# Kernel optimization log

Measured on AMD Instinct MI355X. Metric: run time of the kernel, lower is better.

Reference implementation:

```python
import jax, jax.numpy as jnp
import numpy as np

BS, N_LINKS, MAX_LEN = 8192, 512, 32
D_LINK, D_PATH, D_READ, N_OUT = 32, 128, 256, 3
BN_EPS = 1e-5


def setup_inputs() -> dict:
    key = jax.random.key(0)
    ks = jax.random.split(key, 16)
    capa = jax.random.uniform(ks[0], (BS, N_LINKS), jnp.float32, 0.5, 1.0) * 100.0
    avail = jax.random.uniform(ks[1], (BS, N_LINKS), jnp.float32) * capa
    loss = jax.random.uniform(ks[2], (BS, N_LINKS), jnp.float32) * 0.05
    demand = jax.random.uniform(ks[3], (BS,), jnp.float32) * 10.0
    path = jax.random.randint(ks[4], (BS, MAX_LEN), 0, N_LINKS)
    hop_num = jax.random.randint(ks[5], (BS,), 1, MAX_LEN + 1)
    s = 0.1
    inp = {
        "demand": demand,
        "link_avail_capacity": avail,
        "link_capacity": capa,
        "link_loss": loss,
        "path": path,
        "hop_num": hop_num,
        # GRU params (PyTorch layout: [3H, D] gates ordered r,z,n)
        "gru_w_ih": jax.random.normal(ks[6], (3 * D_PATH, D_LINK), jnp.float32) * s,
        "gru_w_hh": jax.random.normal(ks[7], (3 * D_PATH, D_PATH), jnp.float32) * s,
        "gru_b_ih": jax.random.normal(ks[8], (3 * D_PATH,), jnp.float32) * s,
        "gru_b_hh": jax.random.normal(ks[9], (3 * D_PATH,), jnp.float32) * s,
        "bn_gamma": jnp.ones((D_PATH,), jnp.float32),
        "bn_beta": jnp.zeros((D_PATH,), jnp.float32),
        # stacked readout heads [N_OUT, ...]
        "rW1": jax.random.normal(ks[10], (N_OUT, D_PATH, D_READ), jnp.float32) * s,
        "rb1": jnp.zeros((N_OUT, D_READ), jnp.float32),
        "rW2": jax.random.normal(ks[11], (N_OUT, D_READ, D_READ), jnp.float32) * s,
        "rb2": jnp.zeros((N_OUT, D_READ), jnp.float32),
        "rW3": jax.random.normal(ks[12], (N_OUT, D_READ, 1), jnp.float32) * s,
        "rb3": jnp.zeros((N_OUT, 1), jnp.float32),
    }
    return inp


def _gru_scan(x_bt, h0, w_ih, w_hh, b_ih, b_hh):
    # x_bt: [B, T, D]; h0: [B, H] -> outputs [B, T, H]
    H = h0.shape[-1]
    def step(h, x_t):
        gi = x_t @ w_ih.T + b_ih          # [B, 3H]
        gh = h @ w_hh.T + b_hh            # [B, 3H]
        i_r, i_z, i_n = gi[:, :H], gi[:, H:2*H], gi[:, 2*H:]
        h_r, h_z, h_n = gh[:, :H], gh[:, H:2*H], gh[:, 2*H:]
        r = jax.nn.sigmoid(i_r + h_r)
        z = jax.nn.sigmoid(i_z + h_z)
        n = jnp.tanh(i_n + r * h_n)
        h_new = (1.0 - z) * n + z * h
        return h_new, h_new
    _, outs = jax.lax.scan(step, h0, jnp.swapaxes(x_bt, 0, 1))
    return jnp.swapaxes(outs, 0, 1)


def reference(demand, link_avail_capacity, link_capacity, link_loss, path, hop_num,
              gru_w_ih, gru_w_hh, gru_b_ih, gru_b_hh, bn_gamma, bn_beta,
              rW1, rb1, rW2, rb2, rW3, rb3):
    bs, n_links = link_capacity.shape
    max_len = path.shape[1]
    max_capa = jax.lax.stop_gradient(jnp.max(link_capacity))
    # link_state: [B, n_links, D_LINK]; first D_LINK-4 channels are zeros
    feats = jnp.stack([
        link_avail_capacity / max_capa,
        link_capacity / max_capa,
        link_avail_capacity / link_capacity,
        link_loss,
    ], axis=-1)
    link_state = jnp.concatenate(
        [jnp.zeros((bs, n_links, D_LINK - 4), feats.dtype), feats], axis=-1)
    link_state = jax.lax.stop_gradient(link_state)  # original detaches
    # initial hidden: zeros except last channel = demand/max_capa
    h0 = jnp.concatenate(
        [jnp.zeros((bs, D_PATH - 1), feats.dtype), (demand / max_capa)[:, None]], axis=-1)
    # fused gather of link states along each path, masked past hop_num
    gathered = jnp.take_along_axis(link_state, path[:, :, None], axis=1)  # [B, T, D]
    mask = (jnp.arange(max_len)[None, :] < hop_num[:, None])[:, :, None]
    link_inputs = gathered * mask.astype(gathered.dtype)
    outputs = _gru_scan(link_inputs, h0, gru_w_ih, gru_w_hh, gru_b_ih, gru_b_hh)
    # extract hidden state at last hop of each path
    idx = (hop_num - 1)[:, None, None]
    flow = jnp.take_along_axis(outputs, idx, axis=1)[:, 0, :]  # [B, H]
    # BatchNorm1d (training mode: batch statistics, biased variance)
    mean = jnp.mean(flow, axis=0)
    var = jnp.mean((flow - mean) ** 2, axis=0)
    flow = (flow - mean) * jax.lax.rsqrt(var + BN_EPS) * bn_gamma + bn_beta
    # readout heads: Linear -> SELU -> Linear -> SELU -> Linear
    h1 = jax.nn.selu(jnp.einsum('bh,uhr->ubr', flow, rW1) + rb1[:, None, :])
    h2 = jax.nn.selu(jnp.einsum('ubr,urs->ubs', h1, rW2) + rb2[:, None, :])
    y = jnp.einsum('ubs,uso->ubo', h2, rW3) + rb3[:, None, :]  # [U, B, 1]
    return jnp.transpose(y[:, :, 0], (1, 0))  # [B, U]
```

## Files before the change

kernel.cpp:

```cpp
#include <hip/hip_runtime.h>


#define BS 8192
#define NL 512
#define ML 32
#define DP 128
#define DR 256
#define NJOB 512
#define ST 172

#define OFF_SUM    64
#define OFF_SSQ    192
#define OFF_CUR    576
#define OFF_PERM   640
#define OFF_WHH16  (OFF_PERM + BS)
#define OFF_W1     (OFF_WHH16 + 24576)
#define OFF_W2     (OFF_W1 + 49152)
#define OFF_FEATS  (OFF_W2 + 98304)
#define OFF_FLOW   (OFF_FEATS + BS*ML*4)

#define FEATS_BLOCKS 1024
#define MAX_BLOCKS   256
#define WPREP_BLOCKS 336
#define SORT_BID     (FEATS_BLOCKS + MAX_BLOCKS + WPREP_BLOCKS)
#define PREP_GRID    (SORT_BID + 1)

typedef _Float16 f16x8 __attribute__((ext_vector_type(8)));
typedef _Float16 f16x4 __attribute__((ext_vector_type(4)));
typedef float    f32x4 __attribute__((ext_vector_type(4)));

__device__ __forceinline__ float sigmoidf_(float x){
  return __builtin_amdgcn_rcpf(1.0f + __expf(-x));
}
__device__ __forceinline__ float tanhf_(float x){
  float t = __expf(2.0f*x);
  return 1.0f - 2.0f*__builtin_amdgcn_rcpf(1.0f + t);
}
__device__ __forceinline__ float seluf_(float x){
  const float sc = 1.0507009873554805f, al = 1.6732632423543772f;
  return x > 0.0f ? sc*x : sc*al*(__expf(x)-1.0f);
}

__global__ void prep_all(const int* __restrict__ path, const int* __restrict__ hop,
                         const float* __restrict__ avail, const float* __restrict__ capa,
                         const float* __restrict__ loss, const float* __restrict__ whh,
                         const float* __restrict__ rW1, const float* __restrict__ rW2,
                         float* ws){
  const int bid = blockIdx.x;
  const int tid = threadIdx.x;

  if (bid < FEATS_BLOCKS){
    int idx = bid*256 + tid;
    int b = idx >> 5, t = idx & 31;
    float4 f = make_float4(0.f, 0.f, 0.f, 0.f);
    if (t < hop[b]){
      int l = path[idx];
      float a = avail[b*NL + l];
      float c = capa [b*NL + l];
      f.x = a; f.y = c; f.z = a / c; f.w = loss[b*NL + l];
    }
    ((float4*)(ws + OFF_FEATS))[idx] = f;
  } else if (bid < FEATS_BLOCKS + MAX_BLOCKS){
    const float4* c4 = (const float4*)capa;
    const int n4 = BS*NL/4;
    float m = 0.0f;
    for (int i = (bid - FEATS_BLOCKS)*256 + tid; i < n4; i += MAX_BLOCKS*256){
      float4 v = c4[i];
      m = fmaxf(m, fmaxf(fmaxf(v.x, v.y), fmaxf(v.z, v.w)));
    }
    #pragma unroll
    for (int o = 32; o > 0; o >>= 1) m = fmaxf(m, __shfl_down(m, o, 64));
    if ((tid & 63) == 0) atomicMax((int*)ws, __float_as_int(m));
  } else if (bid < SORT_BID){
    _Float16* whh16 = (_Float16*)(ws + OFF_WHH16);
    _Float16* w1    = (_Float16*)(ws + OFF_W1);
    _Float16* w2    = (_Float16*)(ws + OFF_W2);
    int base = (bid - FEATS_BLOCKS - MAX_BLOCKS)*1024 + tid*4;
    if (base < 49152){
      const float4 v = *(const float4*)(whh + base);
      f16x4 o = { (_Float16)v.x, (_Float16)v.y, (_Float16)v.z, (_Float16)v.w };
      *(f16x4*)(whh16 + base) = o;
    } else if (base < 147456){
      int j = base - 49152; int u = j >> 15; int rem = j & 32767; int n = rem >> 7; int k = rem & 127;
      const float* src = rW1 + u*32768 + k*256 + n;
      f16x4 o = { (_Float16)src[0], (_Float16)src[256], (_Float16)src[512], (_Float16)src[768] };
      *(f16x4*)(w1 + j) = o;
    } else {
      int j = base - 147456; int u = j >> 16; int rem = j & 65535; int n = rem >> 8; int k = rem & 255;
      const float* src = rW2 + u*65536 + k*256 + n;
      f16x4 o = { (_Float16)src[0], (_Float16)src[256], (_Float16)src[512], (_Float16)src[768] };
      *(f16x4*)(w2 + j) = o;
    }
  } else {
    __shared__ int hist[32], start[32];
    for (int i = 64 + tid; i < 640; i += 256) ws[i] = 0.0f;
    if (tid < 32) hist[tid] = 0;
    __syncthreads();
    for (int b = tid; b < BS; b += 256) atomicAdd(&hist[32 - hop[b]], 1);
    __syncthreads();
    if (tid == 0){ int acc = 0; for (int i = 0; i < 32; ++i){ start[i] = acc; acc += hist[i]; } }
    __syncthreads();
    int* perm = (int*)ws + OFF_PERM;
    for (int b = tid; b < BS; b += 256){
      int pos = atomicAdd(&start[32 - hop[b]], 1);
      perm[pos] = b;
    }
  }
}

__launch_bounds__(512, 4)
__global__ void kgru(const float* __restrict__ demand, const int* __restrict__ hop,
                     const float* __restrict__ wih, const float* __restrict__ bih,
                     const float* __restrict__ bhh, float* __restrict__ ws,
                     float* __restrict__ flow){
  __shared__ _Float16 hA[2][16*ST];
  const int tid  = threadIdx.x;
  const int w    = tid >> 6;
  const int lane = tid & 63;
  const int lm   = lane & 15;
  const int qd   = lane >> 4;
  const int ch   = w*16 + lm;
  const float inv_maxc = 1.0f / ws[0];
  const int* perm = (const int*)ws + OFF_PERM;
  const float* feats = ws + OFF_FEATS;
  const _Float16* whh16 = (const _Float16*)(ws + OFF_WHH16);

  const int bid = blockIdx.x;
  const int q = (bid < 256) ? bid : 767 - bid;

  for (int idx = tid; idx < 1024; idx += 512){
    const int buf = idx >> 9;
    const int rem = idx & 511;
    const int m   = rem >> 5;
    const int c   = 128 + (rem & 31);
    hA[buf][m*ST + c] = (_Float16)0.f;
  }

  f16x8 bfr[5], bfz[5], bfnh[4], bfni;
  #pragma unroll
  for (int kc = 0; kc < 4; ++kc){
    bfr[kc]  = *(const f16x8*)(whh16 + (      ch)*128 + kc*32 + qd*8);
    bfz[kc]  = *(const f16x8*)(whh16 + (128 + ch)*128 + kc*32 + qd*8);
    bfnh[kc] = *(const f16x8*)(whh16 + (256 + ch)*128 + kc*32 + qd*8);
  }
  bfr[4] = (f16x8)0; bfz[4] = (f16x8)0; bfni = (f16x8)0;
  if (qd == 0){
    #pragma unroll
    for (int j = 0; j < 4; ++j){
      float s = (j < 2) ? inv_maxc : 1.0f;
      bfr[4][j] = (_Float16)(wih[(      ch)*32 + 28 + j] * s);
      bfz[4][j] = (_Float16)(wih[(128 + ch)*32 + 28 + j] * s);
      bfni[j]   = (_Float16)(wih[(256 + ch)*32 + 28 + j] * s);
    }
  }
  const float bR  = bih[ch]     + bhh[ch];
  const float bZ  = bih[128+ch] + bhh[128+ch];
  const float bNI = bih[256+ch];
  const float bNH = bhh[256+ch];

  int it[4], hp[4];
  #pragma unroll
  for (int r = 0; r < 4; ++r){
    it[r] = perm[q*16 + qd*4 + r];
    hp[r] = hop[it[r]];
  }
  int tmax = max(max(hp[0],hp[1]), max(hp[2],hp[3]));
  tmax = max(tmax, __shfl_xor(tmax, 16, 64));
  tmax = max(tmax, __shfl_xor(tmax, 32, 64));

  const int fw_i = w*2 + (lane >> 2);
  const int fw_c = lane & 3;
  const bool fw  = (lane < 8);
  const int  fw_b = fw ? perm[q*16 + fw_i] : 0;

  __syncthreads();

  float hprev[4];
  #pragma unroll
  for (int r = 0; r < 4; ++r){
    float h0 = (ch == 127) ? demand[it[r]] * inv_maxc : 0.0f;
    hprev[r] = h0;
    hA[0][(qd*4 + r)*ST + ch] = (_Float16)h0;
  }
  if (fw)
    hA[0][fw_i*ST + 128 + fw_c] = (_Float16)feats[(fw_b*ML + 0)*4 + fw_c];
  __syncthreads();

  for (int t = 0; t < tmax; ++t){
    const int cur = t & 1, nxt = cur ^ 1;
    if (fw && (t+1) < ML)
      hA[nxt][fw_i*ST + 128 + fw_c] = (_Float16)feats[(fw_b*ML + t + 1)*4 + fw_c];

    f32x4 accr  = {bR, bR, bR, bR};
    f32x4 accz  = {bZ, bZ, bZ, bZ};
    f32x4 accnh = {bNH, bNH, bNH, bNH};
    f32x4 accni = {bNI, bNI, bNI, bNI};
    #pragma unroll
    for (int kc = 0; kc < 5; ++kc){
      f16x8 a = *(const f16x8*)(&hA[cur][lm*ST + kc*32 + qd*8]);
      accr = __builtin_amdgcn_mfma_f32_16x16x32_f16(a, bfr[kc], accr, 0, 0, 0);
      accz = __builtin_amdgcn_mfma_f32_16x16x32_f16(a, bfz[kc], accz, 0, 0, 0);
      if (kc < 4)
        accnh = __builtin_amdgcn_mfma_f32_16x16x32_f16(a, bfnh[kc], accnh, 0, 0, 0);
      else
        accni = __builtin_amdgcn_mfma_f32_16x16x32_f16(a, bfni, accni, 0, 0, 0);
    }

    #pragma unroll
    for (int r = 0; r < 4; ++r){
      float rr = sigmoidf_(accr[r]);
      float zz = sigmoidf_(accz[r]);
      float nn = tanhf_(fmaf(rr, accnh[r], accni[r]));
      float hn = fmaf(zz, hprev[r] - nn, nn);
      if (t < hp[r]) hprev[r] = hn;
      hA[nxt][(qd*4 + r)*ST + ch] = (_Float16)hprev[r];
    }
    __syncthreads();
  }

  float ssum = 0.f, ssq = 0.f;
  #pragma unroll
  for (int r = 0; r < 4; ++r){
    float v = hprev[r];
    flow[it[r]*DP + ch] = v;
    ssum += v;
    ssq  = fmaf(v, v, ssq);
  }
  ssum += __shfl_xor(ssum, 16, 64);  ssum += __shfl_xor(ssum, 32, 64);
  ssq  += __shfl_xor(ssq,  16, 64);  ssq  += __shfl_xor(ssq,  32, 64);
  if (qd == 0){
    atomicAdd(&ws[OFF_SUM + ch], ssum);
    atomicAdd(&ws[OFF_SSQ + ch], ssq);
  }
}

__launch_bounds__(256, 4)
__global__ void kmlp(const float* __restrict__ flow, const float* __restrict__ ws,
                     const float* __restrict__ gamma, const float* __restrict__ beta,
                     const float* __restrict__ rb1, const float* __restrict__ rb2,
                     const float* __restrict__ rW3, const float* __restrict__ rb3,
                     float* __restrict__ out){
  __shared__ _Float16 x_lds[32*136];
  __shared__ _Float16 h1_lds[32*264];
  __shared__ float aa[DP], bb[DP];
  __shared__ float y_part[4][32];
  const int tid  = threadIdx.x;
  const int w    = tid >> 6;
  const int lane = tid & 63;
  const int lm   = lane & 15;
  const int qd   = lane >> 4;
  const int b0   = blockIdx.x * 32;
  const int u    = blockIdx.y;
  const _Float16* w1 = (const _Float16*)(ws + OFF_W1) + u*(DR*DP);
  const _Float16* w2 = (const _Float16*)(ws + OFF_W2) + u*(DR*DR);

  if (tid < DP){
    float m = ws[OFF_SUM + tid] * (1.0f/BS);
    float q = ws[OFF_SSQ + tid] * (1.0f/BS);
    float rstd = rsqrtf(q - m*m + 1e-5f);
    float a = rstd * gamma[tid];
    aa[tid] = a;
    bb[tid] = fmaf(-m, a, beta[tid]);
  }
  __syncthreads();

  for (int idx = tid; idx < 32*DP; idx += 256){
    int i = idx >> 7, h = idx & 127;
    x_lds[i*136 + h] = (_Float16)fmaf(flow[(b0 + i)*DP + h], aa[h], bb[h]);
  }
  __syncthreads();

  for (int nt = 0; nt < 4; ++nt){
    const int n = (4*w + nt)*16 + lm;
    const float bias1 = rb1[u*DR + n];
    f16x8 b1[4];
    #pragma unroll
    for (int kc = 0; kc < 4; ++kc)
      b1[kc] = *(const f16x8*)(w1 + n*DP + kc*32 + qd*8);
    #pragma unroll
    for (int mt = 0; mt < 2; ++mt){
      f32x4 acc = {bias1, bias1, bias1, bias1};
      #pragma unroll
      for (int kc = 0; kc < 4; ++kc){
        f16x8 a1 = *(const f16x8*)(&x_lds[(mt*16 + lm)*136 + kc*32 + qd*8]);
        acc = __builtin_amdgcn_mfma_f32_16x16x32_f16(a1, b1[kc], acc, 0, 0, 0);
      }
      #pragma unroll
      for (int r = 0; r < 4; ++r)
        h1_lds[(mt*16 + qd*4 + r)*264 + n] = (_Float16)seluf_(acc[r]);
    }
  }
  __syncthreads();

  {
    float p[2][4] = {{0.f,0.f,0.f,0.f},{0.f,0.f,0.f,0.f}};
    for (int nt = 0; nt < 4; ++nt){
      const int n = (4*w + nt)*16 + lm;
      const float bias2 = rb2[u*DR + n];
      const float w3l   = rW3[u*DR + n];
      f16x8 b2[8];
      #pragma unroll
      for (int kc = 0; kc < 8; ++kc)
        b2[kc] = *(const f16x8*)(w2 + n*DR + kc*32 + qd*8);
      #pragma unroll
      for (int mt = 0; mt < 2; ++mt){
        f32x4 acc = {bias2, bias2, bias2, bias2};
        #pragma unroll
        for (int kc = 0; kc < 8; ++kc){
          f16x8 a2 = *(const f16x8*)(&h1_lds[(mt*16 + lm)*264 + kc*32 + qd*8]);
          acc = __builtin_amdgcn_mfma_f32_16x16x32_f16(a2, b2[kc], acc, 0, 0, 0);
        }
        #pragma unroll
        for (int r = 0; r < 4; ++r)
          p[mt][r] += seluf_(acc[r]) * w3l;
      }
    }
    #pragma unroll
    for (int mt = 0; mt < 2; ++mt){
      #pragma unroll
      for (int r = 0; r < 4; ++r){
        float v = p[mt][r];
        v += __shfl_xor(v, 1, 64);
        v += __shfl_xor(v, 2, 64);
        v += __shfl_xor(v, 4, 64);
        v += __shfl_xor(v, 8, 64);
        if (lm == 0) y_part[w][mt*16 + qd*4 + r] = v;
      }
    }
  }
  __syncthreads();
  if (tid < 32){
    float y = y_part[0][tid] + y_part[1][tid] + y_part[2][tid] + y_part[3][tid] + rb3[u];
    out[(b0 + tid)*3 + u] = y;
  }
}

extern "C" void kernel_launch(void* const* d_in, const int* in_sizes, int n_in,
                              void* d_out, int out_size, void* d_ws, size_t ws_size,
                              hipStream_t stream){
  const float* demand = (const float*)d_in[0];
  const float* avail  = (const float*)d_in[1];
  const float* capa   = (const float*)d_in[2];
  const float* loss   = (const float*)d_in[3];
  const int*   path   = (const int*)d_in[4];
  const int*   hop    = (const int*)d_in[5];
  const float* wih    = (const float*)d_in[6];
  const float* whh    = (const float*)d_in[7];
  const float* bih    = (const float*)d_in[8];
  const float* bhh    = (const float*)d_in[9];
  const float* gamma  = (const float*)d_in[10];
  const float* beta   = (const float*)d_in[11];
  const float* rW1    = (const float*)d_in[12];
  const float* rb1    = (const float*)d_in[13];
  const float* rW2    = (const float*)d_in[14];
  const float* rb2    = (const float*)d_in[15];
  const float* rW3    = (const float*)d_in[16];
  const float* rb3    = (const float*)d_in[17];
  float* ws  = (float*)d_ws;
  float* out = (float*)d_out;

  prep_all <<<PREP_GRID, 256, 0, stream>>>(path, hop, avail, capa, loss,
                                           whh, rW1, rW2, ws);
  kgru     <<<NJOB, 512, 0, stream>>>(demand, hop, wih, bih, bhh, ws, ws + OFF_FLOW);
  kmlp     <<<dim3(BS/32, 3), 256, 0, stream>>>(ws + OFF_FLOW, ws, gamma, beta,
                                                rb1, rb2, rW3, rb3, out);
}
```

Measured before the change: 201.2 us.

## Fuse link-feature gather into GRU loop and pre-scale gate weights for exp2

Removes the separate feature-gather blocks from the prep kernel and the intermediate feats buffer. The GRU kernel now reads path indices and the avail/capa/loss values directly, software-pipelined two steps ahead, and computes avail/capa through lane shuffles. Separately, the W_hh, W_ih and bias terms are pre-scaled by -log2(e) or 2·log2(e), so sigmoid and tanh use exp2 directly without an extra multiply. This trades a workspace write and read pass for dependent global loads inside the sequential loop, which may add latency if the prefetch does not hide it.

Measured after the change: 207.0 us. +2.9%, slower.

```diff
diff --git a/kernel.cpp b/kernel.cpp
--- a/kernel.cpp
+++ b/kernel.cpp
@@ -19,22 +19,23 @@
 #define OFF_FEATS  (OFF_W2 + 98304)
 #define OFF_FLOW   (OFF_FEATS + BS*ML*4)
 
-#define FEATS_BLOCKS 1024
 #define MAX_BLOCKS   256
 #define WPREP_BLOCKS 336
-#define SORT_BID     (FEATS_BLOCKS + MAX_BLOCKS + WPREP_BLOCKS)
+#define SORT_BID     (MAX_BLOCKS + WPREP_BLOCKS)
 #define PREP_GRID    (SORT_BID + 1)
+
+#define KS (-1.44269504088896340736f)
+#define KT ( 2.88539008177792681472f)
 
 typedef _Float16 f16x8 __attribute__((ext_vector_type(8)));
 typedef _Float16 f16x4 __attribute__((ext_vector_type(4)));
 typedef float    f32x4 __attribute__((ext_vector_type(4)));
 
-__device__ __forceinline__ float sigmoidf_(float x){
-  return __builtin_amdgcn_rcpf(1.0f + __expf(-x));
-}
-__device__ __forceinline__ float tanhf_(float x){
-  float t = __expf(2.0f*x);
-  return 1.0f - 2.0f*__builtin_amdgcn_rcpf(1.0f + t);
+__device__ __forceinline__ float sig2_(float x){
+  return __builtin_amdgcn_rcpf(1.0f + exp2f(x));
+}
+__device__ __forceinline__ float tanh2_(float v){
+  return fmaf(-2.0f, __builtin_amdgcn_rcpf(1.0f + exp2f(v)), 1.0f);
 }
 __device__ __forceinline__ float seluf_(float x){
   const float sc = 1.0507009873554805f, al = 1.6732632423543772f;
@@ -49,22 +50,11 @@
   const int bid = blockIdx.x;
   const int tid = threadIdx.x;
 
-  if (bid < FEATS_BLOCKS){
-    int idx = bid*256 + tid;
-    int b = idx >> 5, t = idx & 31;
-    float4 f = make_float4(0.f, 0.f, 0.f, 0.f);
-    if (t < hop[b]){
-      int l = path[idx];
-      float a = avail[b*NL + l];
-      float c = capa [b*NL + l];
-      f.x = a; f.y = c; f.z = a / c; f.w = loss[b*NL + l];
-    }
-    ((float4*)(ws + OFF_FEATS))[idx] = f;
-  } else if (bid < FEATS_BLOCKS + MAX_BLOCKS){
+  if (bid < MAX_BLOCKS){
     const float4* c4 = (const float4*)capa;
     const int n4 = BS*NL/4;
     float m = 0.0f;
-    for (int i = (bid - FEATS_BLOCKS)*256 + tid; i < n4; i += MAX_BLOCKS*256){
+    for (int i = bid*256 + tid; i < n4; i += MAX_BLOCKS*256){
       float4 v = c4[i];
       m = fmaxf(m, fmaxf(fmaxf(v.x, v.y), fmaxf(v.z, v.w)));
     }
@@ -75,10 +65,12 @@
     _Float16* whh16 = (_Float16*)(ws + OFF_WHH16);
     _Float16* w1    = (_Float16*)(ws + OFF_W1);
     _Float16* w2    = (_Float16*)(ws + OFF_W2);
-    int base = (bid - FEATS_BLOCKS - MAX_BLOCKS)*1024 + tid*4;
+    int base = (bid - MAX_BLOCKS)*1024 + tid*4;
     if (base < 49152){
+      const float s = (base < 32768) ? KS : KT;
       const float4 v = *(const float4*)(whh + base);
-      f16x4 o = { (_Float16)v.x, (_Float16)v.y, (_Float16)v.z, (_Float16)v.w };
+      f16x4 o = { (_Float16)(v.x*s), (_Float16)(v.y*s),
+                  (_Float16)(v.z*s), (_Float16)(v.w*s) };
       *(f16x4*)(whh16 + base) = o;
     } else if (base < 147456){
       int j = base - 49152; int u = j >> 15; int rem = j & 32767; int n = rem >> 7; int k = rem & 127;
@@ -111,8 +103,10 @@
 __launch_bounds__(512, 4)
 __global__ void kgru(const float* __restrict__ demand, const int* __restrict__ hop,
                      const float* __restrict__ wih, const float* __restrict__ bih,
-                     const float* __restrict__ bhh, float* __restrict__ ws,
-                     float* __restrict__ flow){
+                     const float* __restrict__ bhh,
+                     const float* __restrict__ avail, const float* __restrict__ capa,
+                     const float* __restrict__ loss, const int* __restrict__ path,
+                     float* __restrict__ ws, float* __restrict__ flow){
   __shared__ _Float16 hA[2][16*ST];
   const int tid  = threadIdx.x;
   const int w    = tid >> 6;
@@ -122,7 +116,6 @@
   const int ch   = w*16 + lm;
   const float inv_maxc = 1.0f / ws[0];
   const int* perm = (const int*)ws + OFF_PERM;
-  const float* feats = ws + OFF_FEATS;
   const _Float16* whh16 = (const _Float16*)(ws + OFF_WHH16);
 
   const int bid = blockIdx.x;
@@ -148,15 +141,15 @@
     #pragma unroll
     for (int j = 0; j < 4; ++j){
       float s = (j < 2) ? inv_maxc : 1.0f;
-      bfr[4][j] = (_Float16)(wih[(      ch)*32 + 28 + j] * s);
-      bfz[4][j] = (_Float16)(wih[(128 + ch)*32 + 28 + j] * s);
-      bfni[j]   = (_Float16)(wih[(256 + ch)*32 + 28 + j] * s);
-    }
-  }
-  const float bR  = bih[ch]     + bhh[ch];
-  const float bZ  = bih[128+ch] + bhh[128+ch];
-  const float bNI = bih[256+ch];
-  const float bNH = bhh[256+ch];
+      bfr[4][j] = (_Float16)(wih[(      ch)*32 + 28 + j] * s * KS);
+      bfz[4][j] = (_Float16)(wih[(128 + ch)*32 + 28 + j] * s * KS);
+      bfni[j]   = (_Float16)(wih[(256 + ch)*32 + 28 + j] * s * KT);
+    }
+  }
+  const float bR  = (bih[ch]     + bhh[ch]    ) * KS;
+  const float bZ  = (bih[128+ch] + bhh[128+ch]) * KS;
+  const float bNI = bih[256+ch] * KT;
+  const float bNH = bhh[256+ch] * KT;
 
   int it[4], hp[4];
   #pragma unroll
@@ -168,10 +161,16 @@
   tmax = max(tmax, __shfl_xor(tmax, 16, 64));
   tmax = max(tmax, __shfl_xor(tmax, 32, 64));
 
-  const int fw_i = w*2 + (lane >> 2);
-  const int fw_c = lane & 3;
-  const bool fw  = (lane < 8);
-  const int  fw_b = fw ? perm[q*16 + fw_i] : 0;
+  const int  fw_i = w*2 + (lane >> 2);
+  const int  fw_c = lane & 3;
+  const bool fw   = (lane < 8);
+  const float* pX   = avail;
+  const int*   pPath = path;
+  if (fw){
+    const int fw_b = perm[q*16 + fw_i];
+    pX = ((fw_c == 0) ? avail : (fw_c == 3) ? loss : capa) + fw_b*NL;
+    pPath = path + fw_b*ML;
+  }
 
   __syncthreads();
 
@@ -182,14 +181,33 @@
     hprev[r] = h0;
     hA[0][(qd*4 + r)*ST + ch] = (_Float16)h0;
   }
-  if (fw)
-    hA[0][fw_i*ST + 128 + fw_c] = (_Float16)feats[(fw_b*ML + 0)*4 + fw_c];
+  float rawB = 0.f;
+  int   lA   = 0;
+  if (fw){
+    int l0 = pPath[0];
+    float r0 = pX[l0];
+    float a  = __shfl(r0, lane & ~3, 64);
+    float cc = __shfl(r0, (lane & ~3) | 1, 64);
+    float v0 = (fw_c == 2) ? (a / cc) : r0;
+    hA[0][fw_i*ST + 128 + fw_c] = (_Float16)v0;
+    rawB = pX[pPath[1]];
+    lA   = pPath[2];
+  }
   __syncthreads();
 
   for (int t = 0; t < tmax; ++t){
     const int cur = t & 1, nxt = cur ^ 1;
-    if (fw && (t+1) < ML)
-      hA[nxt][fw_i*ST + 128 + fw_c] = (_Float16)feats[(fw_b*ML + t + 1)*4 + fw_c];
+
+    float rawN = 0.f; int lN = 0;
+    if (fw){
+      rawN = pX[lA];
+      int t3 = t + 3; t3 = (t3 < ML) ? t3 : (ML - 1);
+      lN = pPath[t3];
+      float a  = __shfl(rawB, lane & ~3, 64);
+      float cc = __shfl(rawB, (lane & ~3) | 1, 64);
+      float v  = (fw_c == 2) ? (a / cc) : rawB;
+      hA[nxt][fw_i*ST + 128 + fw_c] = (_Float16)v;
+    }
 
     f32x4 accr  = {bR, bR, bR, bR};
     f32x4 accz  = {bZ, bZ, bZ, bZ};
@@ -208,13 +226,14 @@
 
     #pragma unroll
     for (int r = 0; r < 4; ++r){
-      float rr = sigmoidf_(accr[r]);
-      float zz = sigmoidf_(accz[r]);
-      float nn = tanhf_(fmaf(rr, accnh[r], accni[r]));
+      float rr = sig2_(accr[r]);
+      float zz = sig2_(accz[r]);
+      float nn = tanh2_(fmaf(rr, accnh[r], accni[r]));
       float hn = fmaf(zz, hprev[r] - nn, nn);
       if (t < hp[r]) hprev[r] = hn;
       hA[nxt][(qd*4 + r)*ST + ch] = (_Float16)hprev[r];
     }
+    rawB = rawN; lA = lN;
     __syncthreads();
   }
 
@@ -361,7 +380,8 @@
 
   prep_all <<<PREP_GRID, 256, 0, stream>>>(path, hop, avail, capa, loss,
                                            whh, rW1, rW2, ws);
-  kgru     <<<NJOB, 512, 0, stream>>>(demand, hop, wih, bih, bhh, ws, ws + OFF_FLOW);
+  kgru     <<<NJOB, 512, 0, stream>>>(demand, hop, wih, bih, bhh,
+                                      avail, capa, loss, path, ws, ws + OFF_FLOW);
   kmlp     <<<dim3(BS/32, 3), 256, 0, stream>>>(ws + OFF_FLOW, ws, gamma, beta,
                                                 rb1, rb2, rW3, rb3, out);
 }
```
